# Performance work log

Measured on AMD Instinct MI355X. Metric: run time of the kernel, lower is better.

The kernel has to match this reference:

```python
import jax, jax.numpy as jnp
import numpy as np
from jax import lax

R_MAX = 7  # max per-pixel splat radius: floor(max|defocus|=6) + 1
INT_MIN = np.iinfo(np.int32).min


def setup_inputs() -> dict:
    key = jax.random.key(0)
    k1, k2 = jax.random.split(key)
    B, C, H, W = 4, 3, 512, 1024
    image = jax.random.uniform(k1, (B, C, H, W), dtype=jnp.float32)
    # signed circle-of-confusion (defocus) in pixels
    defocus = jax.random.uniform(k2, (B, 1, H, W), dtype=jnp.float32,
                                 minval=-6.0, maxval=6.0)
    return {"image": image, "defocus": defocus}


def _render(image, defocus):
    """Gather formulation of the per-pixel disk splatting scatter kernel.

    Original CUDA kernel (per source pixel p with radius r=|defocus[p]|,
    intR = int(r)+1) scatters, for every offset (dy,dx) in [-intR,intR]^2:
        w = (0.5 + 0.5*tanh(4*(r - dist))) / max(r*r, 1)
        bokeh_cum[p+o]  += w * image[p]
        weight_cum[p+o] += w
        if dist <= r: defocus_dilate[p+o] = max(., int(defocus[p]))
    Here we flip it into a gather over a fixed offset set of radius R_MAX,
    masking offsets outside each source pixel's square footprint.
    """
    B, C, H, W = image.shape
    P = R_MAX
    r = jnp.abs(defocus)                                   # [B,1,H,W]
    int_r = jnp.floor(r).astype(jnp.int32) + 1             # per-pixel footprint
    def_int = defocus.astype(jnp.int32)                    # trunc toward zero

    pad = ((0, 0), (0, 0), (P, P), (P, P))
    img_p = jnp.pad(image, pad)
    r_p = jnp.pad(r, pad)
    intr_p = jnp.pad(int_r, pad)                           # pad=0 kills pad contributions
    defint_p = jnp.pad(def_int, pad, constant_values=INT_MIN)

    # all offsets of the maximal square footprint
    d = np.arange(-P, P + 1)
    offs = jnp.asarray(np.stack(np.meshgrid(d, d, indexing='ij'), -1)
                       .reshape(-1, 2), dtype=jnp.int32)   # [K,2]

    def step(carry, o):
        bc, wc, dd = carry
        dy, dx = o[0], o[1]
        # source pixel feeding output (y,x) sits at (y-dy, x-dx) -> padded slice
        y0, x0 = P - dy, P - dx
        src_img = lax.dynamic_slice(img_p, (0, 0, y0, x0), (B, C, H, W))
        src_r = lax.dynamic_slice(r_p, (0, 0, y0, x0), (B, 1, H, W))
        src_intr = lax.dynamic_slice(intr_p, (0, 0, y0, x0), (B, 1, H, W))
        src_defint = lax.dynamic_slice(defint_p, (0, 0, y0, x0), (B, 1, H, W))

        dist = jnp.sqrt((dy * dy + dx * dx).astype(jnp.float32))
        in_foot = (jnp.abs(dy) <= src_intr) & (jnp.abs(dx) <= src_intr)
        w = (0.5 + 0.5 * jnp.tanh(4.0 * (src_r - dist))) \
            / jnp.maximum(src_r * src_r, 1.0)
        w = jnp.where(in_foot, w, 0.0)                     # [B,1,H,W]

        bc = bc + w * src_img
        wc = wc + w
        in_circle = in_foot & (dist <= src_r)
        dd = jnp.maximum(dd, jnp.where(in_circle, src_defint, INT_MIN))
        return (bc, wc, dd), None

    init = (jnp.zeros_like(image), jnp.zeros_like(defocus), def_int)
    (bokeh_cum, weight_cum, dd), _ = lax.scan(step, init, offs)

    bokeh = bokeh_cum / weight_cum
    defocus_dilate = dd.astype(jnp.float32)
    return bokeh, defocus_dilate


def reference(image, defocus):
    bokeh, defocus_dilate = _render(image, defocus)
    return bokeh, defocus_dilate
```

## Files before the change

kernel.cpp:

```cpp
#include <hip/hip_runtime.h>
#include <math.h>

#define HH 512
#define WW 1024
#define HWSZ (HH*WW)
#define BB 4
#define KSIG 11.541560327111707
#define DD_OFF (BB*3*HWSZ)

typedef float v2f __attribute__((ext_vector_type(2)));

#define PEVAL(P, MI) {                                                        \
    const float4 t = tp[(MI)*7];                           \
    v2f den = (v2f){t.z, t.w} * rc + rr;                    \
    v2f w = { __builtin_amdgcn_rcpf(den.x),                                   \
              __builtin_amdgcn_rcpf(den.y) };                                 \
    aW##P += w;                                                               \
    aR##P += w * v0;  aG##P += w * v1;  aB##P += w * v2;                      \
    v2f cand = { r >= t.x ? di : -1e30f,                                      \
                 r >= t.y ? di : -1e30f };                                    \
    aD##P = __builtin_elementwise_max(aD##P, cand);                           \
}

#define COLOFF(J)                                                             \
    if (edge) {                                                               \
        const int col = x + (J) - 6;                                          \
        vld = (unsigned)col < (unsigned)WW;                                   \
        const int cc = col < 0 ? 0 : (col > WW-1 ? WW-1 : col);               \
        off = cc - x;                              \
    } else { off = (J) - 6; vld = true; }

#define ROW_SITE(RYY, ...) {                                                  \
    const int sy = y0 + (RYY);                                                \
    if ((unsigned)sy < (unsigned)HH) {          \
        const int rb = sy*WW + x;                                             \
        const float* __restrict__ pd = dP + rb;                               \
        const float* __restrict__ p0 = c0 + rb;                               \
        const float* __restrict__ p1 = c1 + rb;                               \
        const float* __restrict__ p2 = c2 + rb;                               \
        int off; bool vld;                                                    \
        COLOFF(0)                                                             \
        float dcur = pd[off], c0v = p0[off], c1v = p1[off], c2v = p2[off];    \
        if (!vld) dcur = 0.0f;             \
        _Pragma("nounroll")                                                   \
        for (int j = 0; j < 13; ++j) {                                        \
            const int jn = j < 12 ? j + 1 : 12;                               \
            COLOFF(jn)                                                        \
            float dn = pd[off], n0 = p0[off], n1 = p1[off], n2 = p2[off];     \
            if (!vld) dn = 0.0f;                                              \
            const float v0 = c0v, v1 = c1v, v2 = c2v;                         \
            const float r  = fabsf(dcur);                                     \
            const float rr = fmaxf(dcur*dcur, 1.0f);                          \
            const float rc = rr * __builtin_amdgcn_exp2f(r*(float)(-KSIG));   \
            const float di = truncf(dcur);        \
            const int ax = j < 6 ? 6 - j : j - 6;                             \
            const float4* __restrict__ tp = (const float4*)T4 + ax;           \
            __VA_ARGS__                                                       \
            dcur = dn; c0v = n0; c1v = n1; c2v = n2;                          \
        }                                                                     \
    }                                                                         \
}

#define WOUT(P) {                                                             \
    const float ix = __builtin_amdgcn_rcpf(aW##P.x);         \
    const float iy = __builtin_amdgcn_rcpf(aW##P.y);                          \
    const int yA = y0 + 2*(P), yB = yA + 1;                                   \
    const size_t oA = (size_t)yA*WW + x, oB = (size_t)yB*WW + x;              \
    out[(size_t)(b*3+0)*HWSZ + oA] = aR##P.x*ix;                              \
    out[(size_t)(b*3+1)*HWSZ + oA] = aG##P.x*ix;                              \
    out[(size_t)(b*3+2)*HWSZ + oA] = aB##P.x*ix;                              \
    out[DD_OFF + (size_t)b*HWSZ + oA] = aD##P.x;                              \
    out[(size_t)(b*3+0)*HWSZ + oB] = aR##P.y*iy;                              \
    out[(size_t)(b*3+1)*HWSZ + oB] = aG##P.y*iy;                              \
    out[(size_t)(b*3+2)*HWSZ + oB] = aB##P.y*iy;                              \
    out[DD_OFF + (size_t)b*HWSZ + oB] = aD##P.y;                              \
}

__global__ __launch_bounds__(256, 4)
void bokeh_kernel(const float* __restrict__ img,
                  const float* __restrict__ defo,
                  float* __restrict__ out)
{
    __shared__ float4 T4[14][7];
    {
        const int t = threadIdx.x;
        if (t < 14*7) {
            const int mi = t / 7, ax = t - mi*7;
            const int m  = mi - 6;
            const int a0 = m < 0 ? -m : m;
            const int a1 = (m-1) < 0 ? -(m-1) : (m-1);
            float D0 = 1e30f, C0 = __builtin_inff();
            float D1 = 1e30f, C1 = __builtin_inff();
            if (a0 <= 6 && a0*a0 + ax*ax <= 49) {
                D0 = (float)sqrt((double)(a0*a0 + ax*ax));
                C0 = (float)exp2((double)D0 * KSIG);
            }
            if (a1 <= 6 && a1*a1 + ax*ax <= 49) {
                D1 = (float)sqrt((double)(a1*a1 + ax*ax));
                C1 = (float)exp2((double)D1 * KSIG);
            }
            T4[mi][ax] = make_float4(D0, D1, C0, C1);
        }
    }
    __syncthreads();

    const int lane = threadIdx.x & 63;
    const int wv   = threadIdx.x >> 6;
    const int bx   = blockIdx.x;
    const int x    = bx*64 + lane;
    const int y0   = blockIdx.y*32 + wv*8;
    const int b    = blockIdx.z;
    const bool edge = (bx == 0) || (bx == WW/64 - 1);

    const float* __restrict__ dP = defo + (size_t)b*HWSZ;
    const float* __restrict__ c0 = img + (size_t)(b*3+0)*HWSZ;
    const float* __restrict__ c1 = img + (size_t)(b*3+1)*HWSZ;
    const float* __restrict__ c2 = img + (size_t)(b*3+2)*HWSZ;

    v2f aW0={0,0}, aW1={0,0}, aW2={0,0}, aW3={0,0};
    v2f aR0={0,0}, aR1={0,0}, aR2={0,0}, aR3={0,0};
    v2f aG0={0,0}, aG1={0,0}, aG2={0,0}, aG3={0,0};
    v2f aB0={0,0}, aB1={0,0}, aB2={0,0}, aB3={0,0};
    v2f aD0={-1e30f,-1e30f}, aD1={-1e30f,-1e30f};
    v2f aD2={-1e30f,-1e30f}, aD3={-1e30f,-1e30f};

    ROW_SITE(-6, PEVAL(0,0))
    ROW_SITE(-5, PEVAL(0,1))
    ROW_SITE(-4, PEVAL(0,2)  PEVAL(1,0))
    ROW_SITE(-3, PEVAL(0,3)  PEVAL(1,1))
    ROW_SITE(-2, PEVAL(0,4)  PEVAL(1,2)  PEVAL(2,0))
    ROW_SITE(-1, PEVAL(0,5)  PEVAL(1,3)  PEVAL(2,1))
    ROW_SITE( 0, PEVAL(0,6)  PEVAL(1,4)  PEVAL(2,2)  PEVAL(3,0))
    ROW_SITE( 1, PEVAL(0,7)  PEVAL(1,5)  PEVAL(2,3)  PEVAL(3,1))
    ROW_SITE( 2, PEVAL(0,8)  PEVAL(1,6)  PEVAL(2,4)  PEVAL(3,2))
    ROW_SITE( 3, PEVAL(0,9)  PEVAL(1,7)  PEVAL(2,5)  PEVAL(3,3))
    ROW_SITE( 4, PEVAL(0,10) PEVAL(1,8)  PEVAL(2,6)  PEVAL(3,4))
    ROW_SITE( 5, PEVAL(0,11) PEVAL(1,9)  PEVAL(2,7)  PEVAL(3,5))
    ROW_SITE( 6, PEVAL(0,12) PEVAL(1,10) PEVAL(2,8)  PEVAL(3,6))
    ROW_SITE( 7, PEVAL(0,13) PEVAL(1,11) PEVAL(2,9)  PEVAL(3,7))
    ROW_SITE( 8,             PEVAL(1,12) PEVAL(2,10) PEVAL(3,8))
    ROW_SITE( 9,             PEVAL(1,13) PEVAL(2,11) PEVAL(3,9))
    ROW_SITE(10,                         PEVAL(2,12) PEVAL(3,10))
    ROW_SITE(11,                         PEVAL(2,13) PEVAL(3,11))
    ROW_SITE(12,                                     PEVAL(3,12))
    ROW_SITE(13,                                     PEVAL(3,13))

    WOUT(0) WOUT(1) WOUT(2) WOUT(3)
}

extern "C" void kernel_launch(void* const* d_in, const int* in_sizes, int n_in,
                              void* d_out, int out_size, void* d_ws, size_t ws_size,
                              hipStream_t stream)
{
    const float* img  = (const float*)d_in[0];
    const float* defo = (const float*)d_in[1];
    float* out = (float*)d_out;
    bokeh_kernel<<<dim3(WW/64, HH/32, BB), dim3(256,1,1), 0, stream>>>(img, defo, out);
}
```

Baseline: 167.0 us.

## Swap loop nesting to iterate columns outer and unrolled rows inner; branchless dilate max

The per-row column loops become one outer loop over the 13 column offsets. Inside it, all 20 source rows are fully unrolled with clamped row indices instead of branches, so each iteration issues many independent loads and evaluations and there is one loop instead of twenty. The dilation update also changes from compare-and-select to a min, multiply-add and max. The cost is higher register pressure and code size, loss of the software-pipelined prefetch, and loads for out-of-range rows that now happen and are then masked.

New measurement: 159.2 us. 4.7% less time.

```diff
diff --git a/kernel.cpp b/kernel.cpp
--- a/kernel.cpp
+++ b/kernel.cpp
@@ -17,48 +17,24 @@
               __builtin_amdgcn_rcpf(den.y) };                                 \
     aW##P += w;                                                               \
     aR##P += w * v0;  aG##P += w * v1;  aB##P += w * v2;                      \
-    v2f cand = { r >= t.x ? di : -1e30f,                                      \
-                 r >= t.y ? di : -1e30f };                                    \
-    aD##P = __builtin_elementwise_max(aD##P, cand);                           \
+    v2f rd = (v2f){r, r} - (v2f){t.x, t.y};                                   \
+    v2f mdi = __builtin_elementwise_min(rd, (v2f){0.f, 0.f}) * 1e31f + di;    \
+    aD##P = __builtin_elementwise_max(aD##P, mdi);                            \
 }
 
-#define COLOFF(J)                                                             \
-    if (edge) {                                                               \
-        const int col = x + (J) - 6;                                          \
-        vld = (unsigned)col < (unsigned)WW;                                   \
-        const int cc = col < 0 ? 0 : (col > WW-1 ? WW-1 : col);               \
-        off = cc - x;                              \
-    } else { off = (J) - 6; vld = true; }
-
-#define ROW_SITE(RYY, ...) {                                                  \
-    const int sy = y0 + (RYY);                                                \
-    if ((unsigned)sy < (unsigned)HH) {          \
-        const int rb = sy*WW + x;                                             \
-        const float* __restrict__ pd = dP + rb;                               \
-        const float* __restrict__ p0 = c0 + rb;                               \
-        const float* __restrict__ p1 = c1 + rb;                               \
-        const float* __restrict__ p2 = c2 + rb;                               \
-        int off; bool vld;                                                    \
-        COLOFF(0)                                                             \
-        float dcur = pd[off], c0v = p0[off], c1v = p1[off], c2v = p2[off];    \
-        if (!vld) dcur = 0.0f;             \
-        _Pragma("nounroll")                                                   \
-        for (int j = 0; j < 13; ++j) {                                        \
-            const int jn = j < 12 ? j + 1 : 12;                               \
-            COLOFF(jn)                                                        \
-            float dn = pd[off], n0 = p0[off], n1 = p1[off], n2 = p2[off];     \
-            if (!vld) dn = 0.0f;                                              \
-            const float v0 = c0v, v1 = c1v, v2 = c2v;                         \
-            const float r  = fabsf(dcur);                                     \
-            const float rr = fmaxf(dcur*dcur, 1.0f);                          \
-            const float rc = rr * __builtin_amdgcn_exp2f(r*(float)(-KSIG));   \
-            const float di = truncf(dcur);        \
-            const int ax = j < 6 ? 6 - j : j - 6;                             \
-            const float4* __restrict__ tp = (const float4*)T4 + ax;           \
-            __VA_ARGS__                                                       \
-            dcur = dn; c0v = n0; c1v = n1; c2v = n2;                          \
-        }                                                                     \
-    }                                                                         \
+#define ROWV(RYY, ...) {                                                      \
+    const int sy  = y0 + (RYY);                                               \
+    const int scl = sy < 0 ? 0 : (sy > HH-1 ? HH-1 : sy);                     \
+    const bool rv = (unsigned)sy < (unsigned)HH;                              \
+    const int rb  = scl*WW + xoff;                                            \
+    float dv = dP[rb];                                                        \
+    const float v0 = c0[rb], v1 = c1[rb], v2 = c2[rb];                        \
+    dv = (rv && vld) ? dv : 0.0f;                                             \
+    const float r  = fabsf(dv);                                               \
+    const float rr = fmaxf(dv*dv, 1.0f);                                      \
+    const float rc = rr * __builtin_amdgcn_exp2f(r*(float)(-KSIG));           \
+    const float di = truncf(dv);                  \
+    __VA_ARGS__                                                               \
 }
 
 #define WOUT(P) {                                                             \
@@ -124,26 +100,38 @@
     v2f aD0={-1e30f,-1e30f}, aD1={-1e30f,-1e30f};
     v2f aD2={-1e30f,-1e30f}, aD3={-1e30f,-1e30f};
 
-    ROW_SITE(-6, PEVAL(0,0))
-    ROW_SITE(-5, PEVAL(0,1))
-    ROW_SITE(-4, PEVAL(0,2)  PEVAL(1,0))
-    ROW_SITE(-3, PEVAL(0,3)  PEVAL(1,1))
-    ROW_SITE(-2, PEVAL(0,4)  PEVAL(1,2)  PEVAL(2,0))
-    ROW_SITE(-1, PEVAL(0,5)  PEVAL(1,3)  PEVAL(2,1))
-    ROW_SITE( 0, PEVAL(0,6)  PEVAL(1,4)  PEVAL(2,2)  PEVAL(3,0))
-    ROW_SITE( 1, PEVAL(0,7)  PEVAL(1,5)  PEVAL(2,3)  PEVAL(3,1))
-    ROW_SITE( 2, PEVAL(0,8)  PEVAL(1,6)  PEVAL(2,4)  PEVAL(3,2))
-    ROW_SITE( 3, PEVAL(0,9)  PEVAL(1,7)  PEVAL(2,5)  PEVAL(3,3))
-    ROW_SITE( 4, PEVAL(0,10) PEVAL(1,8)  PEVAL(2,6)  PEVAL(3,4))
-    ROW_SITE( 5, PEVAL(0,11) PEVAL(1,9)  PEVAL(2,7)  PEVAL(3,5))
-    ROW_SITE( 6, PEVAL(0,12) PEVAL(1,10) PEVAL(2,8)  PEVAL(3,6))
-    ROW_SITE( 7, PEVAL(0,13) PEVAL(1,11) PEVAL(2,9)  PEVAL(3,7))
-    ROW_SITE( 8,             PEVAL(1,12) PEVAL(2,10) PEVAL(3,8))
-    ROW_SITE( 9,             PEVAL(1,13) PEVAL(2,11) PEVAL(3,9))
-    ROW_SITE(10,                         PEVAL(2,12) PEVAL(3,10))
-    ROW_SITE(11,                         PEVAL(2,13) PEVAL(3,11))
-    ROW_SITE(12,                                     PEVAL(3,12))
-    ROW_SITE(13,                                     PEVAL(3,13))
+#pragma nounroll
+    for (int j = 0; j < 13; ++j) {
+        int xoff; bool vld;
+        if (edge) {
+            const int col = x + j - 6;
+            vld  = (unsigned)col < (unsigned)WW;
+            xoff = col < 0 ? 0 : (col > WW-1 ? WW-1 : col);
+        } else { xoff = x + j - 6; vld = true; }
+        const int ax = j < 6 ? 6 - j : j - 6;
+        const float4* __restrict__ tp = (const float4*)T4 + ax;
+
+        ROWV(-6, PEVAL(0,0))
+        ROWV(-5, PEVAL(0,1))
+        ROWV(-4, PEVAL(0,2)  PEVAL(1,0))
+        ROWV(-3, PEVAL(0,3)  PEVAL(1,1))
+        ROWV(-2, PEVAL(0,4)  PEVAL(1,2)  PEVAL(2,0))
+        ROWV(-1, PEVAL(0,5)  PEVAL(1,3)  PEVAL(2,1))
+        ROWV( 0, PEVAL(0,6)  PEVAL(1,4)  PEVAL(2,2)  PEVAL(3,0))
+        ROWV( 1, PEVAL(0,7)  PEVAL(1,5)  PEVAL(2,3)  PEVAL(3,1))
+        ROWV( 2, PEVAL(0,8)  PEVAL(1,6)  PEVAL(2,4)  PEVAL(3,2))
+        ROWV( 3, PEVAL(0,9)  PEVAL(1,7)  PEVAL(2,5)  PEVAL(3,3))
+        ROWV( 4, PEVAL(0,10) PEVAL(1,8)  PEVAL(2,6)  PEVAL(3,4))
+        ROWV( 5, PEVAL(0,11) PEVAL(1,9)  PEVAL(2,7)  PEVAL(3,5))
+        ROWV( 6, PEVAL(0,12) PEVAL(1,10) PEVAL(2,8)  PEVAL(3,6))
+        ROWV( 7, PEVAL(0,13) PEVAL(1,11) PEVAL(2,9)  PEVAL(3,7))
+        ROWV( 8,             PEVAL(1,12) PEVAL(2,10) PEVAL(3,8))
+        ROWV( 9,             PEVAL(1,13) PEVAL(2,11) PEVAL(3,9))
+        ROWV(10,                         PEVAL(2,12) PEVAL(3,10))
+        ROWV(11,                         PEVAL(2,13) PEVAL(3,11))
+        ROWV(12,                                     PEVAL(3,12))
+        ROWV(13,                                     PEVAL(3,13))
+    }
 
     WOUT(0) WOUT(1) WOUT(2) WOUT(3)
 }
```
